# Performance work log

Hardware: AMD Instinct MI355X
Metric: run time of the kernel (lower is better)

The kernel has to match this reference:

```python
import jax, jax.numpy as jnp
import numpy as np

X_DIM = 20000   # number of input locations (x_l rows)
Y_DIM = 6000    # number of query locations (y_l rows)
REGION_DEG = 10.0  # lon/lat spread so every query has neighbors within 250 km
EARTH_DIAM = 2.0 * 6.378  # thousand-km diameter used by the source
THRESH = 0.25   # 250 km neighborhood threshold


def setup_inputs() -> dict:
    key = jax.random.key(0)
    k1, k2, k3 = jax.random.split(key, 3)
    x = jax.random.normal(k1, (X_DIM, 1), dtype=jnp.float32)
    x_l = jax.random.uniform(k2, (X_DIM, 2), dtype=jnp.float32) * REGION_DEG
    y_l = jax.random.uniform(k3, (Y_DIM, 2), dtype=jnp.float32) * REGION_DEG
    return {"x": x, "x_l": x_l, "y_l": y_l}


def reference(x, x_l, y_l):
    # Training branch of GPR.call, vectorized over the y_dim python loop.
    d2r = jnp.pi / 180.0
    lon_x, lat_x = x_l[:, 0], x_l[:, 1]   # (X,)
    lon_y, lat_y = y_l[:, 0], y_l[:, 1]   # (Y,)
    # haversine terms, shape (Y, X)
    hav = jnp.sin((lat_x[None, :] - lat_y[:, None]) * d2r) ** 2
    hav = hav + (jnp.cos(lat_x * d2r)[None, :] * jnp.cos(lat_y * d2r)[:, None]
                 * jnp.sin((lon_x[None, :] - lon_y[:, None]) * d2r) ** 2)
    d = EARTH_DIAM * jnp.arcsin(jnp.sqrt(hav))  # great-circle distance (thousand km)
    # threshold + gather/scatter in source == masked weights here
    w = jnp.where(d < THRESH, d, 0.0)
    s = jnp.sum(w, axis=1, keepdims=True)        # (Y, 1) per-row normalizer
    L = jnp.where(s > 0, w / jnp.maximum(s, 1e-12), 0.0)  # (Y, X) sparse-ish weights
    m = (L @ x)[:, 0]                            # (Y,) squeezed mean
    # V = 0.001 * I  (noise=None path); returned value is diag_part(V)
    v_diag = jnp.full((y_l.shape[0],), 0.001, dtype=x.dtype)
    return m, v_diag
```

## Files before the change

### kernel.cpp

```cpp
#include <hip/hip_runtime.h>
#include <math.h>


#define TPB    256
#define YPB    4
#define NSTRIP 40
#define NLON   40
#define NCELLS (NSTRIP * NLON)
#define C_CELL   0.25f
#define INV_CELL 4.0f
#define RLAT     1.1250f

__device__ __forceinline__ float sin_poly(float a) {
    float t = a * a;
    return a * fmaf(t, fmaf(t, 8.3333333e-3f, -0.16666667f), 1.0f);
}
__device__ __forceinline__ float cos_poly(float a) {
    float t = a * a;
    return fmaf(t, fmaf(t, fmaf(t, -1.3888889e-3f, 4.1666668e-2f), -0.5f), 1.0f);
}
__device__ __forceinline__ int cell_of(float lon, float lat) {
    int s = (int)(lat * INV_CELL); s = min(max(s, 0), NSTRIP - 1);
    int l = (int)(lon * INV_CELL); l = min(max(l, 0), NLON - 1);
    return s * NLON + l;
}


__global__ __launch_bounds__(TPB) void zero_kernel(int* __restrict__ histX,
                                                   int* __restrict__ histY) {
    for (int i = threadIdx.x; i < NCELLS; i += TPB) { histX[i] = 0; histY[i] = 0; }
}

__global__ __launch_bounds__(TPB) void hist_kernel(
    const float* __restrict__ x_l, const float* __restrict__ y_l,
    int* __restrict__ histX, int* __restrict__ histY, int nx, int ny)
{
    int i = blockIdx.x * TPB + threadIdx.x;
    if (i < nx) {
        atomicAdd(&histX[cell_of(x_l[2 * i], x_l[2 * i + 1])], 1);
    } else if (i < nx + ny) {
        int j = i - nx;
        atomicAdd(&histY[cell_of(y_l[2 * j], y_l[2 * j + 1])], 1);
    }
}

__global__ __launch_bounds__(TPB) void scan_kernel(
    const int* __restrict__ histX, const int* __restrict__ histY,
    int* __restrict__ csX, int* __restrict__ csY,
    int* __restrict__ curX, int* __restrict__ curY)
{
    const int CHUNK = (NCELLS + TPB - 1) / TPB;
    __shared__ int sums[TPB];
    const int* hist      = (blockIdx.x == 0) ? histX : histY;
    int*       cellStart = (blockIdx.x == 0) ? csX  : csY;
    int*       cursor    = (blockIdx.x == 0) ? curX : curY;

    int tid = threadIdx.x;
    int base = tid * CHUNK;
    int local[7];
    int s = 0;
    #pragma unroll
    for (int j = 0; j < CHUNK; ++j) {
        int idx = base + j;
        int v = (idx < NCELLS) ? hist[idx] : 0;
        local[j] = s; s += v;
    }
    sums[tid] = s;
    __syncthreads();
    for (int off = 1; off < TPB; off <<= 1) {
        int t = (tid >= off) ? sums[tid - off] : 0;
        __syncthreads();
        sums[tid] += t;
        __syncthreads();
    }
    int excl = (tid > 0) ? sums[tid - 1] : 0;
    #pragma unroll
    for (int j = 0; j < CHUNK; ++j) {
        int idx = base + j;
        if (idx < NCELLS) { cellStart[idx] = excl + local[j]; cursor[idx] = excl + local[j]; }
    }
    if (tid == TPB - 1) cellStart[NCELLS] = sums[TPB - 1];
}

__global__ __launch_bounds__(TPB) void scatter_kernel(
    const float* __restrict__ x, const float* __restrict__ x_l,
    const float* __restrict__ y_l,
    int* __restrict__ curX, int* __restrict__ curY,
    float4* __restrict__ sortedA, float2* __restrict__ sortedRaw,
    float*  __restrict__ sortedX,
    float2* __restrict__ sortedYL, int* __restrict__ sortedYIdx,
    int nx, int ny)
{
    const float d2r = 0.017453292519943295f;
    int i = blockIdx.x * TPB + threadIdx.x;
    if (i < nx) {
        float lon = x_l[2 * i], lat = x_l[2 * i + 1];
        int pos = atomicAdd(&curX[cell_of(lon, lat)], 1);
        float al = lat * d2r, ao = lon * d2r;
        sortedA[pos]   = make_float4(sin_poly(al), cos_poly(al),
                                     sin_poly(ao), cos_poly(ao));
        sortedRaw[pos] = make_float2(lon, lat);
        sortedX[pos]   = x[i];
    } else if (i < nx + ny) {
        int j = i - nx;
        float lon = y_l[2 * j], lat = y_l[2 * j + 1];
        int pos = atomicAdd(&curY[cell_of(lon, lat)], 1);
        sortedYL[pos]   = make_float2(lon, lat);
        sortedYIdx[pos] = j;
    }
}


__global__ __launch_bounds__(TPB) void gpr_binned(
    const float4* __restrict__ sortedA,
    const float2* __restrict__ sortedRaw,
    const float*  __restrict__ sortedX,
    const int*    __restrict__ cellStart,
    const float2* __restrict__ sortedYL,
    const int*    __restrict__ sortedYIdx,
    float* __restrict__ out, int ny, float Hcut, float HcutM)
{
    const int tid  = threadIdx.x;
    const int wave = tid >> 6;
    const int lane = tid & 63;
    const int j    = blockIdx.x * YPB + wave;

    const float d2r    = 0.017453292519943295f;
    const float r2d    = 57.29577951308232f;
    const float THRESH = 0.25f;
    const float DIAM   = 12.756f;
    const float DIAM6  = 12.756f / 6.0f;
    const float EPS_H  = 5e-8f;

    int   yidx  = 0;
    float lon_y = 0.0f, lat_y = 0.0f;
    if (j < ny) {
        yidx = sortedYIdx[j];
        float2 p = sortedYL[j];
        lon_y = p.x; lat_y = p.y;
    }
    const float sly   = sin_poly(lat_y * d2r);
    const float cly   = cos_poly(lat_y * d2r);
    const float slony = sin_poly(lon_y * d2r);
    const float clony = cos_poly(lon_y * d2r);

    float accw = 0.0f, accwx = 0.0f;

    const int s0 = max(0,          (int)floorf((lat_y - RLAT) * INV_CELL));
    const int s1 = min(NSTRIP - 1, (int)floorf((lat_y + RLAT) * INV_CELL));

    for (int s = s0; s <= s1; ++s) {
        float slo = s * C_CELL, shi = slo + C_CELL;
        float dmin = fmaxf(0.0f, fmaxf(slo - lat_y, lat_y - shi));
        float de   = fmaxf(0.0f, dmin - 3e-3f);
        float sd_  = sin_poly(de * d2r);
        float rem  = HcutM - sd_ * sd_;
        if (rem <= 0.0f) continue;
        float ccm = cos_poly(fminf(shi, 10.0f) * d2r) * cly * 0.999999f;
        float W   = asinf(fminf(1.0f, sqrtf(rem / ccm))) * r2d + 4e-3f;
        int lo = min(NLON - 1, max(0, (int)floorf((lon_y - W) * INV_CELL)));
        int hi = min(NLON - 1, max(0, (int)floorf((lon_y + W) * INV_CELL)));
        int p0 = cellStart[s * NLON + lo];
        int p1 = cellStart[s * NLON + hi + 1];

        for (int k = p0 + lane; k < p1; k += 64) {
            float4 e  = sortedA[k];
            float  xv = sortedX[k];

            float sl  = fmaf(e.x, cly,   -(e.y * sly));
            float sd  = fmaf(e.z, clony, -(e.w * slony));
            float cxy = e.y * cly;
            float hav = fmaf(sl, sl, cxy * (sd * sd));

            float tb  = hav - Hcut;
            float r   = __builtin_amdgcn_sqrtf(hav);
            float d   = r * fmaf(hav, DIAM6, DIAM);

            float w;
            if (__builtin_expect(fabsf(tb) < EPS_H, 0)) {
                float2 raw = sortedRaw[k];
                float lonx = raw.x, latx = raw.y;

                float dlat = __fsub_rn(latx, lat_y);
                float alat = __fmul_rn(dlat, d2r);
                float slf  = (float)sin((double)alat);
                float h1   = __fmul_rn(slf, slf);

                float axl  = __fmul_rn(latx,  d2r);
                float ayl  = __fmul_rn(lat_y, d2r);
                float cxf  = (float)cos((double)axl);
                float cyf  = (float)cos((double)ayl);
                float cc   = __fmul_rn(cxf, cyf);

                float dlon = __fsub_rn(lonx, lon_y);
                float alon = __fmul_rn(dlon, d2r);
                float sdf  = (float)sin((double)alon);
                float h2   = __fmul_rn(sdf, sdf);

                float hv   = __fadd_rn(h1, __fmul_rn(cc, h2));
                float r32  = (float)sqrt((double)hv);
                float as32 = (float)asin((double)r32);
                float dnp  = __fmul_rn(DIAM, as32);
                w = (dnp < THRESH) ? dnp : 0.0f;
            } else {
                w = (tb < 0.0f) ? d : 0.0f;
            }

            accw += w;
            accwx = fmaf(w, xv, accwx);
        }
    }

    #pragma unroll
    for (int off = 32; off > 0; off >>= 1) {
        accw  += __shfl_xor(accw,  off, 64);
        accwx += __shfl_xor(accwx, off, 64);
    }

    if (lane == 0 && j < ny) {
        float m = (accw > 0.0f) ? (accwx / fmaxf(accw, 1e-12f)) : 0.0f;
        out[yidx]      = m;
        out[ny + yidx] = 0.001f;
    }
}


__global__ __launch_bounds__(TPB) void gpr_full(
    const float* __restrict__ x, const float* __restrict__ x_l,
    const float* __restrict__ y_l, float* __restrict__ out,
    int nx, int ny, float Hcut)
{
    __shared__ float4 tA[1024];
    __shared__ float  tX[1024];

    const int tid  = threadIdx.x;
    const int wave = tid >> 6;
    const int lane = tid & 63;
    const int y    = blockIdx.x * YPB + wave;

    const float d2r    = 0.017453292519943295f;
    const float THRESH = 0.25f;
    const float DIAM   = 12.756f;
    const float DIAM6  = 12.756f / 6.0f;
    const float EPS_H  = 5e-8f;

    float lon_y = 0.0f, lat_y = 0.0f;
    if (y < ny) { lon_y = y_l[2 * y]; lat_y = y_l[2 * y + 1]; }
    const float sly   = sin_poly(lat_y * d2r);
    const float cly   = cos_poly(lat_y * d2r);
    const float slony = sin_poly(lon_y * d2r);
    const float clony = cos_poly(lon_y * d2r);

    float accw = 0.0f, accwx = 0.0f;

    const int ntiles = (nx + 1023) / 1024;
    for (int t = 0; t < ntiles; ++t) {
        const int base = t * 1024;
        __syncthreads();
        #pragma unroll
        for (int jj = 0; jj < 1024 / TPB; ++jj) {
            int idx = jj * TPB + tid, i = base + idx;
            if (i < nx) {
                float lon = x_l[2 * i], lat = x_l[2 * i + 1];
                tA[idx] = make_float4(sin_poly(lat * d2r), cos_poly(lat * d2r),
                                      sin_poly(lon * d2r), cos_poly(lon * d2r));
                tX[idx] = x[i];
            }
        }
        __syncthreads();

        const int tn = min(1024, nx - base);
        for (int k = lane; k < tn; k += 64) {
            float4 e  = tA[k];
            float  xv = tX[k];
            float sl  = fmaf(e.x, cly,   -(e.y * sly));
            float sd  = fmaf(e.z, clony, -(e.w * slony));
            float cxy = e.y * cly;
            float hav = fmaf(sl, sl, cxy * (sd * sd));
            float tb  = hav - Hcut;
            float r   = __builtin_amdgcn_sqrtf(hav);
            float d   = r * fmaf(hav, DIAM6, DIAM);
            float w;
            if (__builtin_expect(fabsf(tb) < EPS_H, 0)) {
                int   i    = base + k;
                float lonx = x_l[2 * i], latx = x_l[2 * i + 1];
                float dlat = __fsub_rn(latx, lat_y);
                float alat = __fmul_rn(dlat, d2r);
                float slf  = (float)sin((double)alat);
                float h1   = __fmul_rn(slf, slf);
                float axl  = __fmul_rn(latx,  d2r);
                float ayl  = __fmul_rn(lat_y, d2r);
                float cxf  = (float)cos((double)axl);
                float cyf  = (float)cos((double)ayl);
                float cc   = __fmul_rn(cxf, cyf);
                float dlon = __fsub_rn(lonx, lon_y);
                float alon = __fmul_rn(dlon, d2r);
                float sdf  = (float)sin((double)alon);
                float h2   = __fmul_rn(sdf, sdf);
                float hv   = __fadd_rn(h1, __fmul_rn(cc, h2));
                float r32  = (float)sqrt((double)hv);
                float as32 = (float)asin((double)r32);
                float dnp  = __fmul_rn(DIAM, as32);
                w = (dnp < THRESH) ? dnp : 0.0f;
            } else {
                w = (tb < 0.0f) ? d : 0.0f;
            }
            accw += w;
            accwx = fmaf(w, xv, accwx);
        }
    }

    #pragma unroll
    for (int off = 32; off > 0; off >>= 1) {
        accw  += __shfl_xor(accw,  off, 64);
        accwx += __shfl_xor(accwx, off, 64);
    }

    if (lane == 0 && y < ny) {
        float m = (accw > 0.0f) ? (accwx / fmaxf(accw, 1e-12f)) : 0.0f;
        out[y]      = m;
        out[ny + y] = 0.001f;
    }
}


extern "C" void kernel_launch(void* const* d_in, const int* in_sizes, int n_in,
                              void* d_out, int out_size, void* d_ws, size_t ws_size,
                              hipStream_t stream) {
    const float* x   = (const float*)d_in[0];
    const float* x_l = (const float*)d_in[1];
    const float* y_l = (const float*)d_in[2];
    float* out = (float*)d_out;

    const int nx = in_sizes[0];
    const int ny = in_sizes[2] / 2;

    double th = 0.25 / 12.756;
    double s  = sin(th);
    float Hcut  = (float)(s * s);
    float HcutM = (float)(s * s * 1.001);

    size_t offA   = 0;
    size_t offRaw = offA   + (size_t)nx * sizeof(float4);
    size_t offYL  = offRaw + (size_t)nx * sizeof(float2);
    size_t offX   = offYL  + (size_t)ny * sizeof(float2);
    size_t offYI  = offX   + (size_t)nx * sizeof(float);
    size_t offHX  = offYI  + (size_t)ny * sizeof(int);
    size_t offHY  = offHX  + (size_t)NCELLS * sizeof(int);
    size_t offCSX = offHY  + (size_t)NCELLS * sizeof(int);
    size_t offCSY = offCSX + (size_t)(NCELLS + 1) * sizeof(int);
    size_t offCuX = offCSY + (size_t)(NCELLS + 1) * sizeof(int);
    size_t offCuY = offCuX + (size_t)NCELLS * sizeof(int);
    size_t total  = offCuY + (size_t)NCELLS * sizeof(int);

    const int blocks = (ny + YPB - 1) / YPB;

    if (ws_size >= total) {
        float4* sortedA    = (float4*)((char*)d_ws + offA);
        float2* sortedRaw  = (float2*)((char*)d_ws + offRaw);
        float2* sortedYL   = (float2*)((char*)d_ws + offYL);
        float*  sortedX    = (float*) ((char*)d_ws + offX);
        int*    sortedYIdx = (int*)   ((char*)d_ws + offYI);
        int*    histX      = (int*)   ((char*)d_ws + offHX);
        int*    histY      = (int*)   ((char*)d_ws + offHY);
        int*    csX        = (int*)   ((char*)d_ws + offCSX);
        int*    csY        = (int*)   ((char*)d_ws + offCSY);
        int*    curX       = (int*)   ((char*)d_ws + offCuX);
        int*    curY       = (int*)   ((char*)d_ws + offCuY);

        int nb = (nx + ny + TPB - 1) / TPB;
        zero_kernel<<<1, TPB, 0, stream>>>(histX, histY);
        hist_kernel<<<nb, TPB, 0, stream>>>(x_l, y_l, histX, histY, nx, ny);
        scan_kernel<<<2, TPB, 0, stream>>>(histX, histY, csX, csY, curX, curY);
        scatter_kernel<<<nb, TPB, 0, stream>>>(x, x_l, y_l, curX, curY,
                                               sortedA, sortedRaw, sortedX,
                                               sortedYL, sortedYIdx, nx, ny);
        gpr_binned<<<blocks, TPB, 0, stream>>>(sortedA, sortedRaw, sortedX,
                                               csX, sortedYL, sortedYIdx,
                                               out, ny, Hcut, HcutM);
    } else {
        gpr_full<<<blocks, TPB, 0, stream>>>(x, x_l, y_l, out, nx, ny, Hcut);
    }
}
```

Measured before the change: 91.17 us.

## Fuse prefix scan into scatter kernel and replace zero kernel with memset

Every scatter block now redundantly recomputes the exclusive prefix scan of the histogram into shared memory, so the separate two-block scan launch goes away. Positions are computed as the shared cell start plus an atomic offset on zero-initialized cursors. The zero kernel is replaced by a single hipMemsetAsync over the histogram and cursor region. This removes one launch and one dependency between kernels, at the cost of every block repeating the scan over 1600 cells.

```diff
diff --git a/kernel.cpp b/kernel.cpp
--- a/kernel.cpp
+++ b/kernel.cpp
@@ -4,6 +4,7 @@
 
 #define TPB    256
 #define YPB    4
+#define CH     256
 #define NSTRIP 40
 #define NLON   40
 #define NCELLS (NSTRIP * NLON)
@@ -25,11 +26,6 @@
     return s * NLON + l;
 }
 
-
-__global__ __launch_bounds__(TPB) void zero_kernel(int* __restrict__ histX,
-                                                   int* __restrict__ histY) {
-    for (int i = threadIdx.x; i < NCELLS; i += TPB) { histX[i] = 0; histY[i] = 0; }
-}
 
 __global__ __launch_bounds__(TPB) void hist_kernel(
     const float* __restrict__ x_l, const float* __restrict__ y_l,
@@ -44,18 +40,27 @@
     }
 }
 
-__global__ __launch_bounds__(TPB) void scan_kernel(
+
+__global__ __launch_bounds__(TPB) void scan_scatter(
+    const float* __restrict__ x, const float* __restrict__ x_l,
+    const float* __restrict__ y_l,
     const int* __restrict__ histX, const int* __restrict__ histY,
-    int* __restrict__ csX, int* __restrict__ csY,
-    int* __restrict__ curX, int* __restrict__ curY)
+    int* __restrict__ curX, int* __restrict__ curY,
+    float4* __restrict__ sortedA, float2* __restrict__ sortedRaw,
+    float*  __restrict__ sortedX,
+    float2* __restrict__ sortedYL, int* __restrict__ sortedYIdx,
+    int* __restrict__ csX, int nx, int ny, int nbx)
 {
     const int CHUNK = (NCELLS + TPB - 1) / TPB;
     __shared__ int sums[TPB];
-    const int* hist      = (blockIdx.x == 0) ? histX : histY;
-    int*       cellStart = (blockIdx.x == 0) ? csX  : csY;
-    int*       cursor    = (blockIdx.x == 0) ? curX : curY;
-
-    int tid = threadIdx.x;
+    __shared__ int cs[NCELLS];
+    const int tid = threadIdx.x;
+    const float d2r = 0.017453292519943295f;
+
+    const bool isX = ((int)blockIdx.x < nbx);
+    const int* hist = isX ? histX : histY;
+    int*       cur  = isX ? curX  : curY;
+
     int base = tid * CHUNK;
     int local[7];
     int s = 0;
@@ -77,36 +82,33 @@
     #pragma unroll
     for (int j = 0; j < CHUNK; ++j) {
         int idx = base + j;
-        if (idx < NCELLS) { cellStart[idx] = excl + local[j]; cursor[idx] = excl + local[j]; }
-    }
-    if (tid == TPB - 1) cellStart[NCELLS] = sums[TPB - 1];
-}
-
-__global__ __launch_bounds__(TPB) void scatter_kernel(
-    const float* __restrict__ x, const float* __restrict__ x_l,
-    const float* __restrict__ y_l,
-    int* __restrict__ curX, int* __restrict__ curY,
-    float4* __restrict__ sortedA, float2* __restrict__ sortedRaw,
-    float*  __restrict__ sortedX,
-    float2* __restrict__ sortedYL, int* __restrict__ sortedYIdx,
-    int nx, int ny)
-{
-    const float d2r = 0.017453292519943295f;
-    int i = blockIdx.x * TPB + threadIdx.x;
-    if (i < nx) {
-        float lon = x_l[2 * i], lat = x_l[2 * i + 1];
-        int pos = atomicAdd(&curX[cell_of(lon, lat)], 1);
-        float al = lat * d2r, ao = lon * d2r;
-        sortedA[pos]   = make_float4(sin_poly(al), cos_poly(al),
-                                     sin_poly(ao), cos_poly(ao));
-        sortedRaw[pos] = make_float2(lon, lat);
-        sortedX[pos]   = x[i];
-    } else if (i < nx + ny) {
-        int j = i - nx;
-        float lon = y_l[2 * j], lat = y_l[2 * j + 1];
-        int pos = atomicAdd(&curY[cell_of(lon, lat)], 1);
-        sortedYL[pos]   = make_float2(lon, lat);
-        sortedYIdx[pos] = j;
+        if (idx < NCELLS) {
+            int v = excl + local[j];
+            cs[idx] = v;
+            if (isX && blockIdx.x == 0) csX[idx] = v;
+        }
+    }
+    if (isX && blockIdx.x == 0 && tid == TPB - 1) csX[NCELLS] = sums[TPB - 1];
+    __syncthreads();
+
+    const int bd = isX ? blockIdx.x : blockIdx.x - nbx;
+    const int n  = isX ? nx : ny;
+    int i = bd * CH + tid;
+    if (i < n) {
+        const float* loc = isX ? x_l : y_l;
+        float lon = loc[2 * i], lat = loc[2 * i + 1];
+        int cell = cell_of(lon, lat);
+        int pos = cs[cell] + atomicAdd(&cur[cell], 1);
+        if (isX) {
+            float al = lat * d2r, ao = lon * d2r;
+            sortedA[pos]   = make_float4(sin_poly(al), cos_poly(al),
+                                         sin_poly(ao), cos_poly(ao));
+            sortedRaw[pos] = make_float2(lon, lat);
+            sortedX[pos]   = x[i];
+        } else {
+            sortedYL[pos]   = make_float2(lon, lat);
+            sortedYIdx[pos] = i;
+        }
     }
 }
 
@@ -335,6 +337,9 @@
     const int nx = in_sizes[0];
     const int ny = in_sizes[2] / 2;
 
+    const int nbx = (nx + CH - 1) / CH;
+    const int nby = (ny + CH - 1) / CH;
+
     double th = 0.25 / 12.756;
     double s  = sin(th);
     float Hcut  = (float)(s * s);
@@ -345,13 +350,14 @@
     size_t offYL  = offRaw + (size_t)nx * sizeof(float2);
     size_t offX   = offYL  + (size_t)ny * sizeof(float2);
     size_t offYI  = offX   + (size_t)nx * sizeof(float);
-    size_t offHX  = offYI  + (size_t)ny * sizeof(int);
+    size_t offCSX = offYI  + (size_t)ny * sizeof(int);
+    size_t offZ   = offCSX + (size_t)(NCELLS + 1) * sizeof(int);
+    size_t offHX  = offZ;
     size_t offHY  = offHX  + (size_t)NCELLS * sizeof(int);
-    size_t offCSX = offHY  + (size_t)NCELLS * sizeof(int);
-    size_t offCSY = offCSX + (size_t)(NCELLS + 1) * sizeof(int);
-    size_t offCuX = offCSY + (size_t)(NCELLS + 1) * sizeof(int);
+    size_t offCuX = offHY  + (size_t)NCELLS * sizeof(int);
     size_t offCuY = offCuX + (size_t)NCELLS * sizeof(int);
     size_t total  = offCuY + (size_t)NCELLS * sizeof(int);
+    size_t zbytes = total - offZ;
 
     const int blocks = (ny + YPB - 1) / YPB;
 
@@ -361,20 +367,20 @@
         float2* sortedYL   = (float2*)((char*)d_ws + offYL);
         float*  sortedX    = (float*) ((char*)d_ws + offX);
         int*    sortedYIdx = (int*)   ((char*)d_ws + offYI);
+        int*    csX        = (int*)   ((char*)d_ws + offCSX);
         int*    histX      = (int*)   ((char*)d_ws + offHX);
         int*    histY      = (int*)   ((char*)d_ws + offHY);
-        int*    csX        = (int*)   ((char*)d_ws + offCSX);
-        int*    csY        = (int*)   ((char*)d_ws + offCSY);
         int*    curX       = (int*)   ((char*)d_ws + offCuX);
         int*    curY       = (int*)   ((char*)d_ws + offCuY);
 
+        hipMemsetAsync((char*)d_ws + offZ, 0, zbytes, stream);
         int nb = (nx + ny + TPB - 1) / TPB;
-        zero_kernel<<<1, TPB, 0, stream>>>(histX, histY);
         hist_kernel<<<nb, TPB, 0, stream>>>(x_l, y_l, histX, histY, nx, ny);
-        scan_kernel<<<2, TPB, 0, stream>>>(histX, histY, csX, csY, curX, curY);
-        scatter_kernel<<<nb, TPB, 0, stream>>>(x, x_l, y_l, curX, curY,
-                                               sortedA, sortedRaw, sortedX,
-                                               sortedYL, sortedYIdx, nx, ny);
+        scan_scatter<<<nbx + nby, TPB, 0, stream>>>(x, x_l, y_l,
+                                                    histX, histY, curX, curY,
+                                                    sortedA, sortedRaw, sortedX,
+                                                    sortedYL, sortedYIdx,
+                                                    csX, nx, ny, nbx);
         gpr_binned<<<blocks, TPB, 0, stream>>>(sortedA, sortedRaw, sortedX,
                                                csX, sortedYL, sortedYIdx,
                                                out, ny, Hcut, HcutM);
```

Measured after the change: 93.37 us. 1.02x slower.
